# Performance work log

Measured on AMD Instinct MI355X. Metric: run time of the kernel, lower is better.

Reference implementation:

```python
import jax, jax.numpy as jnp
import numpy as np

B, C, H, W = 32, 1536, 32, 32
M_CLUSTERS, L_DIM, G_DIM = 64, 128, 256
SINKHORN_ITERS = 3
EPS = 1e-12

def setup_inputs() -> dict:
    key = jax.random.key(0)
    ks = jax.random.split(key, 16)
    s = lambda i, shape, scale=0.02: jax.random.normal(ks[i], shape, jnp.float32) * scale
    return {
        'x': jax.random.normal(ks[0], (B, C, H, W), jnp.float32),
        't': jax.random.normal(ks[1], (B, C), jnp.float32),
        'cf_w1': s(2, (512, C)), 'cf_b1': s(3, (512,)),
        'cf_w2': s(4, (L_DIM, 512)), 'cf_b2': s(5, (L_DIM,)),
        'sc_w1': s(6, (512, C)), 'sc_b1': s(7, (512,)),
        'sc_w2': s(8, (M_CLUSTERS, 512)), 'sc_b2': s(9, (M_CLUSTERS,)),
        'tk_w1': s(10, (512, C)), 'tk_b1': s(11, (512,)),
        'tk_w2': s(12, (G_DIM, 512)), 'tk_b2': s(13, (G_DIM,)),
        'dust_bin': jnp.array(1.0, jnp.float32),
    }

def _l2norm(v, axis):
    n = jnp.sqrt(jnp.sum(v * v, axis=axis, keepdims=True))
    return v / jnp.maximum(n, EPS)

def _log_optimal_transport(scores, alpha, iters):
    # scores: [B, m, n]; append dustbin row, run log-space Sinkhorn
    b, m, n = scores.shape
    norm = -jnp.log(jnp.float32(m + n))
    bins = jnp.broadcast_to(alpha, (b, 1, n))
    Z0 = jnp.concatenate([scores, bins], axis=1)             # [B, m+1, n]
    log_mu = jnp.concatenate([jnp.full((m,), norm, jnp.float32),
                              jnp.log(jnp.float32(n - m))[None] + norm])  # [m+1]
    log_nu = jnp.full((n,), norm, jnp.float32)               # [n]
    u = jnp.zeros((b, m + 1), jnp.float32)
    v = jnp.zeros((b, n), jnp.float32)
    for _ in range(iters):
        u = log_mu[None, :] - jax.nn.logsumexp(Z0 + v[:, None, :], axis=2)
        v = log_nu[None, :] - jax.nn.logsumexp(Z0 + u[:, :, None], axis=1)
    return Z0 + u[:, :, None] + v[:, None, :] - norm

def reference(x, t, cf_w1, cf_b1, cf_w2, cf_b2, sc_w1, sc_b1, sc_w2, sc_b2,
              tk_w1, tk_b1, tk_w2, tk_b2, dust_bin):
    b = x.shape[0]
    xf = x.reshape(b, x.shape[1], -1)                        # [B, C, HW]
    # cluster_features: 1x1 conv stack -> [B, l, HW]
    h = jax.nn.relu(jnp.einsum('oc,bcn->bon', cf_w1, xf) + cf_b1[None, :, None])
    f = jnp.einsum('oc,bcn->bon', cf_w2, h) + cf_b2[None, :, None]
    # score: 1x1 conv stack -> [B, m, HW]
    h = jax.nn.relu(jnp.einsum('oc,bcn->bon', sc_w1, xf) + sc_b1[None, :, None])
    p = jnp.einsum('oc,bcn->bon', sc_w2, h) + sc_b2[None, :, None]
    # token_features: MLP -> [B, g]
    tk = jax.nn.relu(t @ tk_w1.T + tk_b1) @ tk_w2.T + tk_b2
    # Sinkhorn OT assignment, drop dustbin row
    p = jnp.exp(_log_optimal_transport(p, dust_bin, SINKHORN_ITERS))[:, :-1, :]  # [B, m, HW]
    # fused VLAD aggregation (avoids the repeat-materialized tensors)
    agg = jnp.einsum('bln,bmn->blm', f, p)                   # [B, l, m]
    agg = _l2norm(agg, axis=1).reshape(b, -1)                # [B, l*m]
    v = jnp.concatenate([_l2norm(tk, axis=-1), agg], axis=-1)
    return _l2norm(v, axis=-1)
```

## Files before the change

### kernel.cpp

```cpp
#include <hip/hip_runtime.h>
#include <hip/hip_bf16.h>
#include <math.h>

typedef unsigned short u16;
typedef __attribute__((ext_vector_type(8))) short short8;
typedef __attribute__((ext_vector_type(4))) float floatx4;

#define DEVINL __device__ __forceinline__

DEVINL float bf2f(u16 u) { union { unsigned int i; float f; } v; v.i = ((unsigned int)u) << 16; return v.f; }
DEVINL u16 f2bf(float f) {
  union { unsigned int i; float f; } v; v.f = f;
  unsigned int i = v.i;
  unsigned int r = (i + 0x7fffu + ((i >> 16) & 1u)) >> 16;
  return (u16)r;
}

__global__ __launch_bounds__(256) void k_cvt(const float* __restrict__ src,
                                             u16* __restrict__ dst, int n4) {
  int i = blockIdx.x * 256 + threadIdx.x;
  if (i >= n4) return;
  float4 v = ((const float4*)src)[i];
  ushort4 o;
  o.x = f2bf(v.x); o.y = f2bf(v.y); o.z = f2bf(v.z); o.w = f2bf(v.w);
  ((ushort4*)dst)[i] = o;
}

__global__ __launch_bounds__(256) void k_transpose(const float* __restrict__ x,
                                                   u16* __restrict__ xT,
                                                   int nC, int nN) {
  __shared__ u16 tile[64 * 65];
  int b = blockIdx.z;
  int c0 = blockIdx.y * 64, n0 = blockIdx.x * 64;
  const float* xb = x + ((long)b * nC + c0) * nN + n0;
  u16* xTb = xT + ((long)b * nN + n0) * nC + c0;
  int tid = threadIdx.x;
#pragma unroll
  for (int p = 0; p < 2; ++p) {
    int u = tid + p * 256;
    int r = u >> 3, nc = (u & 7) * 8;
    const float4* srcp = (const float4*)(xb + (long)r * nN + nc);
    float4 v0 = srcp[0], v1 = srcp[1];
    int base = r * 65 + nc;
    tile[base + 0] = f2bf(v0.x); tile[base + 1] = f2bf(v0.y);
    tile[base + 2] = f2bf(v0.z); tile[base + 3] = f2bf(v0.w);
    tile[base + 4] = f2bf(v1.x); tile[base + 5] = f2bf(v1.y);
    tile[base + 6] = f2bf(v1.z); tile[base + 7] = f2bf(v1.w);
  }
  __syncthreads();
#pragma unroll
  for (int p = 0; p < 2; ++p) {
    int u = tid + p * 256;
    int nr = u >> 3, cc = (u & 7) * 8;
    __align__(16) u16 tmp[8];
#pragma unroll
    for (int j = 0; j < 8; ++j) tmp[j] = tile[(cc + j) * 65 + nr];
    *(uint4*)(xTb + (long)nr * nC + cc) = *(uint4*)(tmp);
  }
}

template <bool OUT_F32, int BIAS_MODE, bool RELU>
__global__ __launch_bounds__(256) void k_gemm_bt(
    const u16* __restrict__ A, int lda, long aBS,
    const u16* __restrict__ B1, const u16* __restrict__ B2, int nSplit,
    int ldb, long bBS,
    void* __restrict__ Out, int ldo, long oBS,
    const float* __restrict__ bias1, const float* __restrict__ bias2,
    int M, int N, int K) {
  __shared__ __align__(16) u16 As[128 * 32];
  __shared__ __align__(16) u16 Bs[128 * 32];
  int bz = blockIdx.z;
  int m0 = blockIdx.y * 128, n0 = blockIdx.x * 128;
  const u16* Ablk = A + (long)bz * aBS + (long)m0 * lda;
  const u16* Bblk =
      ((n0 < nSplit) ? (B1 + (long)n0 * ldb) : (B2 + (long)(n0 - nSplit) * ldb)) +
      (long)bz * bBS;
  int tid = threadIdx.x;
  int lane = tid & 63;
  int lane16 = lane & 15, quad = lane >> 4;
  int wid = tid >> 6;
  int wm = wid >> 1, wn = wid & 1;

  int rA0 = (lane >> 2);
  int kk = (lane & 3) * 8;
  int mMax = M - 1 - m0, nMax = N - 1 - n0;

  floatx4 acc[4][4];
#pragma unroll
  for (int i = 0; i < 4; ++i)
#pragma unroll
    for (int j = 0; j < 4; ++j) acc[i][j] = (floatx4){0.f, 0.f, 0.f, 0.f};

  for (int k0 = 0; k0 < K; k0 += 32) {
    __syncthreads();
#pragma unroll
    for (int h = 0; h < 2; ++h) {
      int ch = wid * 2 + h;
      int r = ch * 16 + rA0;
      int ra = min(r, mMax);
      const u16* srcA = Ablk + (long)ra * lda + k0 + kk;
      __builtin_amdgcn_global_load_lds(
          (const __attribute__((address_space(1))) void*)srcA,
          (__attribute__((address_space(3))) void*)&As[ch * 512], 16, 0, 0);
      int rb = min(r, nMax);
      const u16* srcB = Bblk + (long)rb * ldb + k0 + kk;
      __builtin_amdgcn_global_load_lds(
          (const __attribute__((address_space(1))) void*)srcB,
          (__attribute__((address_space(3))) void*)&Bs[ch * 512], 16, 0, 0);
    }
    __syncthreads();
    short8 af[4], bfr[4];
#pragma unroll
    for (int t = 0; t < 4; ++t)
      af[t] = *(const short8*)&As[(wm * 64 + t * 16 + lane16) * 32 + quad * 8];
#pragma unroll
    for (int t = 0; t < 4; ++t)
      bfr[t] = *(const short8*)&Bs[(wn * 64 + t * 16 + lane16) * 32 + quad * 8];
#pragma unroll
    for (int i = 0; i < 4; ++i)
#pragma unroll
      for (int j = 0; j < 4; ++j)
        acc[i][j] = __builtin_amdgcn_mfma_f32_16x16x32_bf16(af[i], bfr[j],
                                                            acc[i][j], 0, 0, 0);
  }

  const float* bcolPtr = bias1;
  int bofs = 0;
  if (BIAS_MODE == 2 && n0 >= nSplit) { bcolPtr = bias2; bofs = nSplit; }
#pragma unroll
  for (int i = 0; i < 4; ++i) {
    int rowb = m0 + wm * 64 + i * 16 + quad * 4;
#pragma unroll
    for (int j = 0; j < 4; ++j) {
      int col = n0 + wn * 64 + j * 16 + lane16;
      if (col >= N) continue;
      float bc = 0.f;
      if (BIAS_MODE == 2) bc = bcolPtr[col - bofs];
#pragma unroll
      for (int r = 0; r < 4; ++r) {
        int row = rowb + r;
        if (row >= M) continue;
        float v = acc[i][j][r];
        if (BIAS_MODE == 2) v += bc;
        if (BIAS_MODE == 1) v += bias1[row];
        if (RELU) v = fmaxf(v, 0.f);
        if (OUT_F32)
          ((float*)Out)[(long)bz * oBS + (long)row * ldo + col] = v;
        else
          ((u16*)Out)[(long)bz * oBS + (long)row * ldo + col] = f2bf(v);
      }
    }
  }
}

__global__ __launch_bounds__(1024) void k_sinkhorn(
    const u16* __restrict__ S, const float* __restrict__ alphaPtr,
    float lmu, float lmu_bin, float lnu, float norm, u16* __restrict__ P) {
  __shared__ float u_[65];
  __shared__ float v_[1024];
  int b = blockIdx.x, tid = threadIdx.x;
  const u16* Sb = S + (long)b * 65536;
  float alpha = *alphaPtr;
  v_[tid] = 0.f;
  __syncthreads();
  int wid = tid >> 6, lane = tid & 63;
  for (int it = 0; it < 3; ++it) {
    for (int i = wid; i < 65; i += 16) {
      float vals[16];
      float mx = -3.4e38f;
#pragma unroll
      for (int s = 0; s < 16; ++s) {
        int j = lane + s * 64;
        float z = (i < 64 ? bf2f(Sb[i * 1024 + j]) : alpha) + v_[j];
        vals[s] = z;
        mx = fmaxf(mx, z);
      }
#pragma unroll
      for (int off = 32; off > 0; off >>= 1) mx = fmaxf(mx, __shfl_xor(mx, off));
      float sum = 0.f;
#pragma unroll
      for (int s = 0; s < 16; ++s) sum += __expf(vals[s] - mx);
#pragma unroll
      for (int off = 32; off > 0; off >>= 1) sum += __shfl_xor(sum, off);
      if (lane == 0) u_[i] = (i < 64 ? lmu : lmu_bin) - (mx + __logf(sum));
    }
    __syncthreads();
    {
      float mx = -3.4e38f, sum = 0.f;
      for (int i = 0; i < 65; ++i) {
        float z = (i < 64 ? bf2f(Sb[i * 1024 + tid]) : alpha) + u_[i];
        if (z > mx) { sum = sum * __expf(mx - z) + 1.f; mx = z; }
        else sum += __expf(z - mx);
      }
      v_[tid] = lnu - (mx + __logf(sum));
    }
    __syncthreads();
  }
  float vj = v_[tid];
  u16* Pb = P + (long)b * 65536;
  for (int i = 0; i < 64; ++i) {
    float z = bf2f(Sb[i * 1024 + tid]) + u_[i] + vj - norm;
    Pb[i * 1024 + tid] = f2bf(__expf(fminf(z, 1.0f)));
  }
}

__global__ __launch_bounds__(256) void k_agg(const u16* __restrict__ f,
                                             const u16* __restrict__ P,
                                             float* __restrict__ aggP) {
  __shared__ __align__(16) u16 Fs[128 * 32];
  __shared__ __align__(16) u16 Ps[64 * 32];
  int bz = blockIdx.z, kc = blockIdx.x;
  const u16* Fb = f + (long)bz * 128 * 1024;
  const u16* Pb = P + (long)bz * 64 * 1024;
  int tid = threadIdx.x, wid = tid >> 6, lane = tid & 63;
  int lane16 = lane & 15, quad = lane >> 4;
  int rA0 = lane >> 2, kk = (lane & 3) * 8;

  floatx4 acc[2][4];
#pragma unroll
  for (int i = 0; i < 2; ++i)
#pragma unroll
    for (int j = 0; j < 4; ++j) acc[i][j] = (floatx4){0.f, 0.f, 0.f, 0.f};

  for (int k0 = kc * 256; k0 < kc * 256 + 256; k0 += 32) {
    __syncthreads();
#pragma unroll
    for (int h = 0; h < 2; ++h) {
      int ch = wid * 2 + h;
      int r = ch * 16 + rA0;
      const u16* srcF = Fb + (long)r * 1024 + k0 + kk;
      __builtin_amdgcn_global_load_lds(
          (const __attribute__((address_space(1))) void*)srcF,
          (__attribute__((address_space(3))) void*)&Fs[ch * 512], 16, 0, 0);
    }
    {
      int r = wid * 16 + rA0;
      const u16* srcP = Pb + (long)r * 1024 + k0 + kk;
      __builtin_amdgcn_global_load_lds(
          (const __attribute__((address_space(1))) void*)srcP,
          (__attribute__((address_space(3))) void*)&Ps[wid * 512], 16, 0, 0);
    }
    __syncthreads();
    short8 af[2], bfr[4];
#pragma unroll
    for (int t = 0; t < 2; ++t)
      af[t] = *(const short8*)&Fs[(wid * 32 + t * 16 + lane16) * 32 + quad * 8];
#pragma unroll
    for (int j = 0; j < 4; ++j)
      bfr[j] = *(const short8*)&Ps[(j * 16 + lane16) * 32 + quad * 8];
#pragma unroll
    for (int i = 0; i < 2; ++i)
#pragma unroll
      for (int j = 0; j < 4; ++j)
        acc[i][j] = __builtin_amdgcn_mfma_f32_16x16x32_bf16(af[i], bfr[j],
                                                            acc[i][j], 0, 0, 0);
  }
  float* ab = aggP + ((long)kc * 32 + bz) * 8192;
#pragma unroll
  for (int i = 0; i < 2; ++i)
#pragma unroll
    for (int j = 0; j < 4; ++j)
#pragma unroll
      for (int r = 0; r < 4; ++r) {
        int row = wid * 32 + i * 16 + quad * 4 + r;
        int col = j * 16 + lane16;
        ab[row * 64 + col] = acc[i][j][r];
      }
}

DEVINL float waveSum(float x) {
#pragma unroll
  for (int off = 32; off > 0; off >>= 1) x += __shfl_xor(x, off);
  return x;
}

__global__ __launch_bounds__(256) void k_mlp1(const float* __restrict__ t,
                                              const float* __restrict__ w1,
                                              const float* __restrict__ b1,
                                              float* __restrict__ h1) {
  __shared__ float tl[1536];
  int b = blockIdx.y, og = blockIdx.x;
  int tid = threadIdx.x, wid = tid >> 6, lane = tid & 63;
  for (int i = tid; i < 1536; i += 256) tl[i] = t[b * 1536 + i];
  __syncthreads();
#pragma unroll 4
  for (int oi = 0; oi < 16; ++oi) {
    int o = og * 64 + wid * 16 + oi;
    const float* wr = w1 + (long)o * 1536;
    float acc = 0.f;
#pragma unroll
    for (int s = 0; s < 24; ++s) { int c = lane + s * 64; acc += tl[c] * wr[c]; }
    acc = waveSum(acc);
    if (lane == 0) h1[b * 512 + o] = fmaxf(acc + b1[o], 0.f);
  }
}

__global__ __launch_bounds__(256) void k_mlp2(const float* __restrict__ h1,
                                              const float* __restrict__ w2,
                                              const float* __restrict__ b2,
                                              float* __restrict__ tk) {
  __shared__ float hl[512];
  int b = blockIdx.y, og = blockIdx.x;
  int tid = threadIdx.x, wid = tid >> 6, lane = tid & 63;
  for (int i = tid; i < 512; i += 256) hl[i] = h1[b * 512 + i];
  __syncthreads();
#pragma unroll 4
  for (int oi = 0; oi < 16; ++oi) {
    int o = og * 64 + wid * 16 + oi;
    const float* wr = w2 + (long)o * 512;
    float acc = 0.f;
#pragma unroll
    for (int s = 0; s < 8; ++s) { int c = lane + s * 64; acc += hl[c] * wr[c]; }
    acc = waveSum(acc);
    if (lane == 0) tk[b * 256 + o] = acc + b2[o];
  }
}

DEVINL float blockSum256(float x, float* red) {
#pragma unroll
  for (int off = 32; off > 0; off >>= 1) x += __shfl_xor(x, off);
  int wid = threadIdx.x >> 6;
  __syncthreads();
  if ((threadIdx.x & 63) == 0) red[wid] = x;
  __syncthreads();
  return red[0] + red[1] + red[2] + red[3];
}

__global__ __launch_bounds__(256) void k_norms(const float* __restrict__ tk,
                                               const float* __restrict__ aggP,
                                               float* __restrict__ out) {
  __shared__ float asum[8192];
  __shared__ float cn[64];
  __shared__ float red[4];
  int b = blockIdx.x, tid = threadIdx.x;
  const float* a0 = aggP + (long)b * 8192;
  for (int idx = tid; idx < 8192; idx += 256)
    asum[idx] = a0[idx] + a0[32 * 8192 + idx] + a0[64 * 8192 + idx] +
                a0[96 * 8192 + idx];
  __syncthreads();
  float tkv = tk[b * 256 + tid];
  float tss = blockSum256(tkv * tkv, red);
  float tn = fmaxf(sqrtf(tss), 1e-12f);
  if (tid < 64) {
    float s = 0.f;
    for (int l = 0; l < 128; ++l) { float a = asum[l * 64 + tid]; s += a * a; }
    cn[tid] = fmaxf(sqrtf(s), 1e-12f);
  }
  __syncthreads();
  float gs = (tkv / tn) * (tkv / tn);
  for (int idx = tid; idx < 8192; idx += 256) {
    float a = asum[idx] / cn[idx & 63];
    gs += a * a;
  }
  float G = blockSum256(gs, red);
  float inv = 1.f / fmaxf(sqrtf(G), 1e-12f);
  float* ob = out + (long)b * 8448;
  ob[tid] = tkv / tn * inv;
  for (int idx = tid; idx < 8192; idx += 256)
    ob[256 + idx] = asum[idx] / cn[idx & 63] * inv;
}

extern "C" void kernel_launch(void* const* d_in, const int* in_sizes, int n_in,
                              void* d_out, int out_size, void* d_ws,
                              size_t ws_size, hipStream_t stream) {
  const float* x = (const float*)d_in[0];
  const float* t = (const float*)d_in[1];
  const float* cf_w1 = (const float*)d_in[2];
  const float* cf_b1 = (const float*)d_in[3];
  const float* cf_w2 = (const float*)d_in[4];
  const float* cf_b2 = (const float*)d_in[5];
  const float* sc_w1 = (const float*)d_in[6];
  const float* sc_b1 = (const float*)d_in[7];
  const float* sc_w2 = (const float*)d_in[8];
  const float* sc_b2 = (const float*)d_in[9];
  const float* tk_w1 = (const float*)d_in[10];
  const float* tk_b1 = (const float*)d_in[11];
  const float* tk_w2 = (const float*)d_in[12];
  const float* tk_b2 = (const float*)d_in[13];
  const float* dust = (const float*)d_in[14];
  float* out = (float*)d_out;

  char* ws = (char*)d_ws;
  size_t off = 0;
  u16* wc1 = (u16*)(ws + off); off += (size_t)512 * 1536 * 2;
  u16* ws1 = (u16*)(ws + off); off += (size_t)512 * 1536 * 2;
  u16* wc2 = (u16*)(ws + off); off += (size_t)128 * 512 * 2;
  u16* ws2 = (u16*)(ws + off); off += (size_t)64 * 512 * 2;
  u16* f = (u16*)(ws + off);   off += (size_t)32 * 128 * 1024 * 2;
  u16* scr = (u16*)(ws + off); off += (size_t)32 * 64 * 1024 * 2;
  u16* P = (u16*)(ws + off);   off += (size_t)32 * 64 * 1024 * 2;
  float* aggP = (float*)(ws + off); off += (size_t)4 * 32 * 128 * 64 * 4;
  float* h1ws = (float*)(ws + off); off += (size_t)32 * 512 * 4;
  float* tkws = (float*)(ws + off); off += (size_t)32 * 256 * 4;
  size_t fixed = off;
  size_t perB = (size_t)1024 * 1536 * 2 + (size_t)1024 * 1024 * 2;
  int c = 1;
  const int cands[6] = {32, 16, 8, 4, 2, 1};
  for (int k = 0; k < 6; ++k)
    if (fixed + (size_t)cands[k] * perB <= ws_size) { c = cands[k]; break; }
  u16* xT = (u16*)(ws + fixed);
  u16* hT = (u16*)(ws + fixed + (size_t)c * 1024 * 1536 * 2);

  k_cvt<<<768, 256, 0, stream>>>(cf_w1, wc1, 512 * 1536 / 4);
  k_cvt<<<768, 256, 0, stream>>>(sc_w1, ws1, 512 * 1536 / 4);
  k_cvt<<<64, 256, 0, stream>>>(cf_w2, wc2, 128 * 512 / 4);
  k_cvt<<<32, 256, 0, stream>>>(sc_w2, ws2, 64 * 512 / 4);

  k_mlp1<<<dim3(8, 32), 256, 0, stream>>>(t, tk_w1, tk_b1, h1ws);
  k_mlp2<<<dim3(4, 32), 256, 0, stream>>>(h1ws, tk_w2, tk_b2, tkws);

  float norm = -logf(1088.f);
  float lmu = norm;
  float lmu_bin = logf(960.f) + norm;
  float lnu = norm;

  for (int cb = 0; cb < 32; cb += c) {
    k_transpose<<<dim3(16, 24, c), 256, 0, stream>>>(
        x + (size_t)cb * 1536 * 1024, xT, 1536, 1024);
    k_gemm_bt<false, 2, true><<<dim3(8, 8, c), 256, 0, stream>>>(
        xT, 1536, (long)1024 * 1536,
        wc1, ws1, 512, 1536, 0,
        hT, 1024, (long)1024 * 1024,
        cf_b1, sc_b1, 1024, 1024, 1536);
    k_gemm_bt<false, 1, false><<<dim3(8, 1, c), 256, 0, stream>>>(
        wc2, 512, 0,
        hT, hT, 1 << 30, 1024, (long)1024 * 1024,
        f + (size_t)cb * 128 * 1024, 1024, (long)128 * 1024,
        cf_b2, cf_b2, 128, 1024, 512);
    k_gemm_bt<false, 1, false><<<dim3(8, 1, c), 256, 0, stream>>>(
        ws2, 512, 0,
        hT + 512, hT + 512, 1 << 30, 1024, (long)1024 * 1024,
        scr + (size_t)cb * 64 * 1024, 1024, (long)64 * 1024,
        sc_b2, sc_b2, 64, 1024, 512);
  }
  k_sinkhorn<<<32, 1024, 0, stream>>>(scr, dust, lmu, lmu_bin, lnu, norm, P);
  k_agg<<<dim3(4, 1, 32), 256, 0, stream>>>(f, P, aggP);
  k_norms<<<32, 256, 0, stream>>>(tkws, aggP, out);
}
```

Before: 679.7 us.

## Use BK=64 swizzled LDS tiles in GEMM and pad score weights to 128 rows

The GEMM now stages 64-wide K slices with an XOR-swizzled LDS layout, which halves the number of barrier pairs per K step and is meant to avoid LDS bank conflicts. The M/N bounds clamps and checks are dropped; to keep that safe, the 64-row score weight and bias are zero-padded to 128 rows, and the score buffer stride doubles to match. The Sinkhorn column pass replaces the online logsumexp with a two-pass max-then-sum and adds unrolling. In exchange, the padded score GEMM does extra work and the sinkhorn reads S twice per column pass.

Measured after the change: 638.6 us. 1.06x faster.

```diff
diff --git a/kernel.cpp b/kernel.cpp
--- a/kernel.cpp
+++ b/kernel.cpp
@@ -24,6 +24,23 @@
   ushort4 o;
   o.x = f2bf(v.x); o.y = f2bf(v.y); o.z = f2bf(v.z); o.w = f2bf(v.w);
   ((ushort4*)dst)[i] = o;
+}
+
+__global__ __launch_bounds__(256) void k_pad_scw2(const float* __restrict__ src,
+                                                  u16* __restrict__ dst) {
+  int i = blockIdx.x * 256 + threadIdx.x;
+  int r = i >> 7;
+  ushort4 o = {0, 0, 0, 0};
+  if (r < 64) {
+    float4 v = ((const float4*)src)[i];
+    o.x = f2bf(v.x); o.y = f2bf(v.y); o.z = f2bf(v.z); o.w = f2bf(v.w);
+  }
+  ((ushort4*)dst)[i] = o;
+}
+
+__global__ void k_pad_scb2(const float* __restrict__ src, float* __restrict__ dst) {
+  int i = threadIdx.x;
+  dst[i] = (i < 64) ? src[i] : 0.f;
 }
 
 __global__ __launch_bounds__(256) void k_transpose(const float* __restrict__ x,
@@ -60,15 +77,15 @@
 }
 
 template <bool OUT_F32, int BIAS_MODE, bool RELU>
-__global__ __launch_bounds__(256) void k_gemm_bt(
+__global__ __launch_bounds__(256) void k_gemm64(
     const u16* __restrict__ A, int lda, long aBS,
     const u16* __restrict__ B1, const u16* __restrict__ B2, int nSplit,
     int ldb, long bBS,
     void* __restrict__ Out, int ldo, long oBS,
     const float* __restrict__ bias1, const float* __restrict__ bias2,
     int M, int N, int K) {
-  __shared__ __align__(16) u16 As[128 * 32];
-  __shared__ __align__(16) u16 Bs[128 * 32];
+  __shared__ __align__(16) u16 As[128 * 64];
+  __shared__ __align__(16) u16 Bs[128 * 64];
   int bz = blockIdx.z;
   int m0 = blockIdx.y * 128, n0 = blockIdx.x * 128;
   const u16* Ablk = A + (long)bz * aBS + (long)m0 * lda;
@@ -81,9 +98,8 @@
   int wid = tid >> 6;
   int wm = wid >> 1, wn = wid & 1;
 
-  int rA0 = (lane >> 2);
-  int kk = (lane & 3) * 8;
-  int mMax = M - 1 - m0, nMax = N - 1 - n0;
+  int rIn = lane >> 3;
+  int kkSw = ((lane & 7) ^ rIn) * 8;
 
   floatx4 acc[4][4];
 #pragma unroll
@@ -91,37 +107,42 @@
 #pragma unroll
     for (int j = 0; j < 4; ++j) acc[i][j] = (floatx4){0.f, 0.f, 0.f, 0.f};
 
-  for (int k0 = 0; k0 < K; k0 += 32) {
-    __syncthreads();
-#pragma unroll
-    for (int h = 0; h < 2; ++h) {
-      int ch = wid * 2 + h;
-      int r = ch * 16 + rA0;
-      int ra = min(r, mMax);
-      const u16* srcA = Ablk + (long)ra * lda + k0 + kk;
+  for (int k0 = 0; k0 < K; k0 += 64) {
+    __syncthreads();
+#pragma unroll
+    for (int h = 0; h < 4; ++h) {
+      int ch = wid * 4 + h;
+      int r = ch * 8 + rIn;
+      const u16* srcA = Ablk + (long)r * lda + k0 + kkSw;
       __builtin_amdgcn_global_load_lds(
           (const __attribute__((address_space(1))) void*)srcA,
           (__attribute__((address_space(3))) void*)&As[ch * 512], 16, 0, 0);
-      int rb = min(r, nMax);
-      const u16* srcB = Bblk + (long)rb * ldb + k0 + kk;
+      const u16* srcB = Bblk + (long)r * ldb + k0 + kkSw;
       __builtin_amdgcn_global_load_lds(
           (const __attribute__((address_space(1))) void*)srcB,
           (__attribute__((address_space(3))) void*)&Bs[ch * 512], 16, 0, 0);
     }
     __syncthreads();
-    short8 af[4], bfr[4];
-#pragma unroll
-    for (int t = 0; t < 4; ++t)
-      af[t] = *(const short8*)&As[(wm * 64 + t * 16 + lane16) * 32 + quad * 8];
-#pragma unroll
-    for (int t = 0; t < 4; ++t)
-      bfr[t] = *(const short8*)&Bs[(wn * 64 + t * 16 + lane16) * 32 + quad * 8];
-#pragma unroll
-    for (int i = 0; i < 4; ++i)
-#pragma unroll
-      for (int j = 0; j < 4; ++j)
-        acc[i][j] = __builtin_amdgcn_mfma_f32_16x16x32_bf16(af[i], bfr[j],
-                                                            acc[i][j], 0, 0, 0);
+#pragma unroll
+    for (int h2 = 0; h2 < 2; ++h2) {
+      short8 af[4], bfr[4];
+#pragma unroll
+      for (int t = 0; t < 4; ++t) {
+        int ra = wm * 64 + t * 16 + lane16;
+        af[t] = *(const short8*)&As[ra * 64 + (((h2 * 4 + quad) ^ (ra & 7)) * 8)];
+      }
+#pragma unroll
+      for (int t = 0; t < 4; ++t) {
+        int rb = wn * 64 + t * 16 + lane16;
+        bfr[t] = *(const short8*)&Bs[rb * 64 + (((h2 * 4 + quad) ^ (rb & 7)) * 8)];
+      }
+#pragma unroll
+      for (int i = 0; i < 4; ++i)
+#pragma unroll
+        for (int j = 0; j < 4; ++j)
+          acc[i][j] = __builtin_amdgcn_mfma_f32_16x16x32_bf16(af[i], bfr[j],
+                                                              acc[i][j], 0, 0, 0);
+    }
   }
 
   const float* bcolPtr = bias1;
@@ -133,13 +154,11 @@
 #pragma unroll
     for (int j = 0; j < 4; ++j) {
       int col = n0 + wn * 64 + j * 16 + lane16;
-      if (col >= N) continue;
       float bc = 0.f;
       if (BIAS_MODE == 2) bc = bcolPtr[col - bofs];
 #pragma unroll
       for (int r = 0; r < 4; ++r) {
         int row = rowb + r;
-        if (row >= M) continue;
         float v = acc[i][j][r];
         if (BIAS_MODE == 2) v += bc;
         if (BIAS_MODE == 1) v += bias1[row];
@@ -159,7 +178,7 @@
   __shared__ float u_[65];
   __shared__ float v_[1024];
   int b = blockIdx.x, tid = threadIdx.x;
-  const u16* Sb = S + (long)b * 65536;
+  const u16* Sb = S + (long)b * 131072;
   float alpha = *alphaPtr;
   v_[tid] = 0.f;
   __syncthreads();
@@ -186,18 +205,21 @@
     }
     __syncthreads();
     {
-      float mx = -3.4e38f, sum = 0.f;
-      for (int i = 0; i < 65; ++i) {
-        float z = (i < 64 ? bf2f(Sb[i * 1024 + tid]) : alpha) + u_[i];
-        if (z > mx) { sum = sum * __expf(mx - z) + 1.f; mx = z; }
-        else sum += __expf(z - mx);
-      }
+      float mx = alpha + u_[64];
+#pragma unroll 8
+      for (int i = 0; i < 64; ++i)
+        mx = fmaxf(mx, bf2f(Sb[i * 1024 + tid]) + u_[i]);
+      float sum = __expf(alpha + u_[64] - mx);
+#pragma unroll 8
+      for (int i = 0; i < 64; ++i)
+        sum += __expf(bf2f(Sb[i * 1024 + tid]) + u_[i] - mx);
       v_[tid] = lnu - (mx + __logf(sum));
     }
     __syncthreads();
   }
   float vj = v_[tid];
   u16* Pb = P + (long)b * 65536;
+#pragma unroll 8
   for (int i = 0; i < 64; ++i) {
     float z = bf2f(Sb[i * 1024 + tid]) + u_[i] + vj - norm;
     Pb[i * 1024 + tid] = f2bf(__expf(fminf(z, 1.0f)));
@@ -385,9 +407,10 @@
   u16* wc1 = (u16*)(ws + off); off += (size_t)512 * 1536 * 2;
   u16* ws1 = (u16*)(ws + off); off += (size_t)512 * 1536 * 2;
   u16* wc2 = (u16*)(ws + off); off += (size_t)128 * 512 * 2;
-  u16* ws2 = (u16*)(ws + off); off += (size_t)64 * 512 * 2;
+  u16* ws2p = (u16*)(ws + off); off += (size_t)128 * 512 * 2;
+  float* scb2p = (float*)(ws + off); off += (size_t)128 * 4;
   u16* f = (u16*)(ws + off);   off += (size_t)32 * 128 * 1024 * 2;
-  u16* scr = (u16*)(ws + off); off += (size_t)32 * 64 * 1024 * 2;
+  u16* scr = (u16*)(ws + off); off += (size_t)32 * 128 * 1024 * 2;
   u16* P = (u16*)(ws + off);   off += (size_t)32 * 64 * 1024 * 2;
   float* aggP = (float*)(ws + off); off += (size_t)4 * 32 * 128 * 64 * 4;
   float* h1ws = (float*)(ws + off); off += (size_t)32 * 512 * 4;
@@ -404,7 +427,8 @@
   k_cvt<<<768, 256, 0, stream>>>(cf_w1, wc1, 512 * 1536 / 4);
   k_cvt<<<768, 256, 0, stream>>>(sc_w1, ws1, 512 * 1536 / 4);
   k_cvt<<<64, 256, 0, stream>>>(cf_w2, wc2, 128 * 512 / 4);
-  k_cvt<<<32, 256, 0, stream>>>(sc_w2, ws2, 64 * 512 / 4);
+  k_pad_scw2<<<64, 256, 0, stream>>>(sc_w2, ws2p);
+  k_pad_scb2<<<1, 128, 0, stream>>>(sc_b2, scb2p);
 
   k_mlp1<<<dim3(8, 32), 256, 0, stream>>>(t, tk_w1, tk_b1, h1ws);
   k_mlp2<<<dim3(4, 32), 256, 0, stream>>>(h1ws, tk_w2, tk_b2, tkws);
@@ -417,21 +441,21 @@
   for (int cb = 0; cb < 32; cb += c) {
     k_transpose<<<dim3(16, 24, c), 256, 0, stream>>>(
         x + (size_t)cb * 1536 * 1024, xT, 1536, 1024);
-    k_gemm_bt<false, 2, true><<<dim3(8, 8, c), 256, 0, stream>>>(
+    k_gemm64<false, 2, true><<<dim3(8, 8, c), 256, 0, stream>>>(
         xT, 1536, (long)1024 * 1536,
         wc1, ws1, 512, 1536, 0,
         hT, 1024, (long)1024 * 1024,
         cf_b1, sc_b1, 1024, 1024, 1536);
-    k_gemm_bt<false, 1, false><<<dim3(8, 1, c), 256, 0, stream>>>(
+    k_gemm64<false, 1, false><<<dim3(8, 1, c), 256, 0, stream>>>(
         wc2, 512, 0,
         hT, hT, 1 << 30, 1024, (long)1024 * 1024,
         f + (size_t)cb * 128 * 1024, 1024, (long)128 * 1024,
         cf_b2, cf_b2, 128, 1024, 512);
-    k_gemm_bt<false, 1, false><<<dim3(8, 1, c), 256, 0, stream>>>(
-        ws2, 512, 0,
+    k_gemm64<false, 1, false><<<dim3(8, 1, c), 256, 0, stream>>>(
+        ws2p, 512, 0,
         hT + 512, hT + 512, 1 << 30, 1024, (long)1024 * 1024,
-        scr + (size_t)cb * 64 * 1024, 1024, (long)64 * 1024,
-        sc_b2, sc_b2, 64, 1024, 512);
+        scr + (size_t)cb * 128 * 1024, 1024, (long)128 * 1024,
+        scb2p, scb2p, 128, 1024, 512);
   }
   k_sinkhorn<<<32, 1024, 0, stream>>>(scr, dust, lmu, lmu_bin, lnu, norm, P);
   k_agg<<<dim3(4, 1, 32), 256, 0, stream>>>(f, P, aggP);
```
